# Performance work log

Hardware: AMD Instinct MI355X
Metric: run time of the kernel (lower is better)

The kernel has to match this reference:

```python
import jax, jax.numpy as jnp
import numpy as np


def setup_inputs() -> dict:
    key = jax.random.key(0)
    ks = jax.random.split(key, 8)
    B, C, H, W = 4, 512, 64, 64
    M = C // 8
    sq = 1.0 / np.sqrt(C)
    return {
        "x": jax.random.normal(ks[0], (B, C, H, W), jnp.float32),
        "Wq": jax.random.normal(ks[1], (M, C), jnp.float32) * sq,
        "bq": jnp.zeros((M,), jnp.float32),
        "Wk": jax.random.normal(ks[2], (M, C), jnp.float32) * sq,
        "bk": jnp.zeros((M,), jnp.float32),
        "Wv": jax.random.normal(ks[3], (C, C), jnp.float32) * sq,
        "bv": jnp.zeros((C,), jnp.float32),
        "gamma": jax.random.uniform(ks[4], (1,), jnp.float32),
    }


def reference(x, Wq, bq, Wk, bk, Wv, bv, gamma):
    B, C, H, W = x.shape
    N = H * W
    xf = x.reshape(B, C, N)  # flatten spatial -> [B, C, N]
    # 1x1 convs are channel-mixing matmuls
    q = jnp.einsum('mc,bcn->bmn', Wq, xf) + bq[None, :, None]  # [B, M, N]
    k = jnp.einsum('mc,bcn->bmn', Wk, xf) + bk[None, :, None]  # [B, M, N]
    v = jnp.einsum('dc,bcn->bdn', Wv, xf) + bv[None, :, None]  # [B, C, N]
    # sim[b,i,j] = <q[:, i], k[:, j]>, softmax over j
    sim = jnp.einsum('bmi,bmj->bij', q, k)  # [B, N, N]
    attn = jax.nn.softmax(sim, axis=-1)
    # feat[b,c,i] = sum_j v[b,c,j] * attn[b,i,j]
    feat = jnp.einsum('bcj,bij->bci', v, attn)  # [B, C, N]
    out = gamma[0] * feat.reshape(B, C, H, W) + x
    return out
```

## Files before the change

### kernel.cpp

```cpp
#include <hip/hip_runtime.h>

typedef _Float16 f16;
typedef _Float16 f16x8 __attribute__((ext_vector_type(8)));
typedef float    f32x4 __attribute__((ext_vector_type(4)));
typedef unsigned int u32x2 __attribute__((ext_vector_type(2)));

#define B_ 4
#define C_ 512
#define N_ 4096
#define M_ 64

__device__ __forceinline__ unsigned pk2(float a, float b) {
    union { f16 h[2]; unsigned u; } t;
    t.h[0] = (f16)a; t.h[1] = (f16)b;
    return t.u;
}

__global__ __launch_bounds__(256) void wcvt(
    const float* __restrict__ Wq, const float* __restrict__ Wk,
    const float* __restrict__ Wv, f16* __restrict__ Wf)
{
    const int e = (blockIdx.x * 256 + threadIdx.x) * 8;
    const float* src;
    int off;
    if (e < 32768)      { src = Wq; off = e; }
    else if (e < 65536) { src = Wk; off = e - 32768; }
    else                { src = Wv; off = e - 65536; }
    float4 a = *(const float4*)(src + off);
    float4 b = *(const float4*)(src + off + 4);
    f16x8 o;
    o[0]=(f16)a.x; o[1]=(f16)a.y; o[2]=(f16)a.z; o[3]=(f16)a.w;
    o[4]=(f16)b.x; o[5]=(f16)b.y; o[6]=(f16)b.z; o[7]=(f16)b.w;
    *(f16x8*)(Wf + e) = o;
}

__global__ __launch_bounds__(512) void qkv2(
    const f16* __restrict__ Wf, const float* __restrict__ x,
    const float* __restrict__ bq, const float* __restrict__ bk,
    const float* __restrict__ bv,
    f16* __restrict__ qt, f16* __restrict__ ktf, f16* __restrict__ vf)
{
    __shared__ __align__(16) char sH[2][8192];
    __shared__ float sBias[640];

    const int tid  = threadIdx.x;
    const int w    = tid >> 6;
    const int lane = tid & 63;
    const int l15  = lane & 15;
    const int quad = lane >> 4;
    const int n0   = blockIdx.x * 64;
    const int b    = blockIdx.y;
    const int row0 = w * 80;

    for (int e = tid; e < 640; e += 512)
        sBias[e] = (e < 64) ? bq[e] : (e < 128) ? bk[e - 64] : bv[e - 128];

    const int wbyte = (lane * 128 + w * 16) ^ ((lane & 7) << 4);
    int rbyte[4][2];
    #pragma unroll
    for (int nt = 0; nt < 4; ++nt) {
        const int n = nt * 16 + l15;
        #pragma unroll
        for (int kh = 0; kh < 2; ++kh)
            rbyte[nt][kh] = (n * 128 + kh * 64 + quad * 16) ^ ((n & 7) << 4);
    }

    const float* xg = x + (size_t)b * (C_ * N_) + n0 + lane;
    const f16*   wp = Wf + (size_t)row0 * 512 + quad * 8;

    {
        float g[8];
        #pragma unroll
        for (int u = 0; u < 8; ++u)
            g[u] = xg[(size_t)(w * 8 + u) * N_];
        f16x8 h;
        #pragma unroll
        for (int u = 0; u < 8; ++u) h[u] = (f16)g[u];
        *(f16x8*)(&sH[0][0] + wbyte) = h;
    }
    f16x8 afc[5][2];
    #pragma unroll
    for (int ot = 0; ot < 5; ++ot)
        #pragma unroll
        for (int kh = 0; kh < 2; ++kh)
            afc[ot][kh] = *(const f16x8*)(wp + (size_t)(ot * 16 + l15) * 512 + kh * 32);

    f32x4 acc[5][4] = {};

    for (int t = 0; t < 8; ++t) {
        char* sc = &sH[t & 1][0];
        char* sn = &sH[(t & 1) ^ 1][0];

        float gn[8];
        f16x8 afn[5][2];
        if (t < 7) {
            #pragma unroll
            for (int u = 0; u < 8; ++u)
                gn[u] = xg[(size_t)((t + 1) * 64 + w * 8 + u) * N_];
            #pragma unroll
            for (int ot = 0; ot < 5; ++ot)
                #pragma unroll
                for (int kh = 0; kh < 2; ++kh)
                    afn[ot][kh] = *(const f16x8*)(wp + (size_t)(ot * 16 + l15) * 512
                                                  + (t + 1) * 64 + kh * 32);
        }

        __syncthreads();

        f16x8 bf[4][2];
        #pragma unroll
        for (int nt = 0; nt < 4; ++nt)
            #pragma unroll
            for (int kh = 0; kh < 2; ++kh)
                bf[nt][kh] = *(const f16x8*)(sc + rbyte[nt][kh]);

        #pragma unroll
        for (int ot = 0; ot < 5; ++ot)
            #pragma unroll
            for (int kh = 0; kh < 2; ++kh)
                #pragma unroll
                for (int nt = 0; nt < 4; ++nt)
                    acc[ot][nt] = __builtin_amdgcn_mfma_f32_16x16x32_f16(
                        afc[ot][kh], bf[nt][kh], acc[ot][nt], 0, 0, 0);

        if (t < 7) {
            f16x8 h;
            #pragma unroll
            for (int u = 0; u < 8; ++u) h[u] = (f16)gn[u];
            *(f16x8*)(sn + wbyte) = h;
            #pragma unroll
            for (int ot = 0; ot < 5; ++ot)
                #pragma unroll
                for (int kh = 0; kh < 2; ++kh)
                    afc[ot][kh] = afn[ot][kh];
        }
    }

    #pragma unroll
    for (int ot = 0; ot < 5; ++ot) {
        const int rowBase = row0 + ot * 16;
        const int rq = rowBase + quad * 4;
        #pragma unroll
        for (int nt = 0; nt < 4; ++nt) {
            const int n = n0 + nt * 16 + l15;
            union { f16 h[4]; unsigned long long u; } pkv;
            #pragma unroll
            for (int r = 0; r < 4; ++r)
                pkv.h[r] = (f16)(acc[ot][nt][r] + sBias[rq + r]);
            if (rowBase < 64) {
                *(unsigned long long*)(qt + ((size_t)(b * N_ + n)) * M_ + rq) = pkv.u;
            } else if (rowBase < 128) {
                const int ol = rq - 64;
                size_t idx = (((size_t)b * 256 + (n >> 4)) * 2 + (ol >> 5)) * 512
                           + (size_t)((((ol >> 3) & 3) * 16 + (n & 15)) * 8) + (ol & 7);
                *(unsigned long long*)(ktf + idx) = pkv.u;
            } else {
                const int c = rq - 128;
                #pragma unroll
                for (int r = 0; r < 4; ++r) {
                    size_t idx = ((size_t)b * (C_ * N_)) + (size_t)((c + r) >> 4) * 65536
                               + (size_t)(n >> 6) * 1024 + (size_t)((n >> 5) & 1) * 512
                               + (size_t)((((n >> 3) & 3) * 16 + ((c + r) & 15)) * 8) + (n & 7);
                    vf[idx] = pkv.h[r];
                }
            }
        }
    }
}

__global__ __launch_bounds__(512, 2) void attn(
    const f16* __restrict__ qt, const f16* __restrict__ ktf,
    const f16* __restrict__ vf, const float* __restrict__ x,
    const float* __restrict__ gamma, float* __restrict__ out)
{
    __shared__ __align__(16) char Pb[2][8192];
    __shared__ float mxs[8][4][16];
    __shared__ float lss[8][4][16];

    const int tid  = threadIdx.x;
    const int w    = tid >> 6;
    const int lane = tid & 63;
    const int l15  = lane & 15;
    const int quad = lane >> 4;
    const int jt   = w & 3;
    const int ish  = w >> 2;
    const int is0  = ish * 2, is1 = is0 + 1;

    const int lin  = blockIdx.x;
    const int b    = (lin & 7) >> 1;
    const int iblk = ((lin >> 3) << 1) | (lin & 1);
    const int i0   = iblk * 64;

    const f16* kln = ktf + (size_t)b * (N_ * M_) + lane * 8;
    const f16* vln = vf  + (size_t)b * (C_ * N_) + lane * 8;

    f16x8 bqf[4][2];
    #pragma unroll
    for (int is = 0; is < 4; ++is)
        #pragma unroll
        for (int kh = 0; kh < 2; ++kh)
            bqf[is][kh] = *(const f16x8*)(qt + ((size_t)(b * N_ + i0 + is * 16 + l15)) * M_
                                          + kh * 32 + quad * 8);

    float mx[4];
    #pragma unroll
    for (int is = 0; is < 4; ++is) mx[is] = -3.0e38f;
    {
        const f16* kw = kln + (size_t)(w * 512) * 64;
        f16x8 akc[4][2];
        #pragma unroll
        for (int t = 0; t < 4; ++t)
            #pragma unroll
            for (int kh = 0; kh < 2; ++kh)
                akc[t][kh] = *(const f16x8*)(kw + t * 1024 + kh * 512);

        #pragma unroll 2
        for (int jj = 0; jj < 512; jj += 64) {
            f16x8 akn[4][2];
            if (jj + 64 < 512) {
                const f16* kn = kw + (size_t)(jj + 64) * 64;
                #pragma unroll
                for (int t = 0; t < 4; ++t)
                    #pragma unroll
                    for (int kh = 0; kh < 2; ++kh)
                        akn[t][kh] = *(const f16x8*)(kn + t * 1024 + kh * 512);
            }
            #pragma unroll
            for (int t = 0; t < 4; ++t) {
                #pragma unroll
                for (int is = 0; is < 4; ++is) {
                    f32x4 s = {};
                    s = __builtin_amdgcn_mfma_f32_16x16x32_f16(akc[t][0], bqf[is][0], s, 0, 0, 0);
                    s = __builtin_amdgcn_mfma_f32_16x16x32_f16(akc[t][1], bqf[is][1], s, 0, 0, 0);
                    mx[is] = fmaxf(mx[is], fmaxf(fmaxf(s[0], s[1]), fmaxf(s[2], s[3])));
                }
            }
            #pragma unroll
            for (int t = 0; t < 4; ++t)
                #pragma unroll
                for (int kh = 0; kh < 2; ++kh)
                    akc[t][kh] = akn[t][kh];
        }
    }
    #pragma unroll
    for (int is = 0; is < 4; ++is) {
        mx[is] = fmaxf(mx[is], __shfl_xor(mx[is], 16, 64));
        mx[is] = fmaxf(mx[is], __shfl_xor(mx[is], 32, 64));
    }
    if (lane < 16) {
        #pragma unroll
        for (int is = 0; is < 4; ++is) mxs[w][is][lane] = mx[is];
    }
    __syncthreads();
    float m0 = -3.0e38f, m1 = -3.0e38f;
    #pragma unroll
    for (int w2 = 0; w2 < 8; ++w2) {
        m0 = fmaxf(m0, mxs[w2][is0][l15]);
        m1 = fmaxf(m1, mxs[w2][is1][l15]);
    }

    f32x4 acc[4][4] = {};
    float lp0 = 0.f, lp1 = 0.f;

    char* pbB = (char*)&Pb[0][0];
    const int swz = (l15 & 7) << 4;
    const int wb0 = ((is0 * 16 + l15) * 128 + (jt * 16 + quad * 4) * 2) ^ swz;
    const int wb1 = wb0 + 2048;
    int rb[4][2];
    #pragma unroll
    for (int is = 0; is < 4; ++is)
        #pragma unroll
        for (int kh = 0; kh < 2; ++kh)
            rb[is][kh] = ((is * 16 + l15) * 128 + kh * 64 + quad * 16) ^ swz;

    const f16* kp = kln + (size_t)(jt * 16) * 64;
    const int cw = w * 4;

    f16x8 ak0 = *(const f16x8*)(kp);
    f16x8 ak1 = *(const f16x8*)(kp + 512);
    {
        f32x4 s0 = {}, s1 = {};
        s0 = __builtin_amdgcn_mfma_f32_16x16x32_f16(ak0, bqf[is0][0], s0, 0, 0, 0);
        s0 = __builtin_amdgcn_mfma_f32_16x16x32_f16(ak1, bqf[is0][1], s0, 0, 0, 0);
        s1 = __builtin_amdgcn_mfma_f32_16x16x32_f16(ak0, bqf[is1][0], s1, 0, 0, 0);
        s1 = __builtin_amdgcn_mfma_f32_16x16x32_f16(ak1, bqf[is1][1], s1, 0, 0, 0);
        float p0 = __expf(s0[0] - m0), p1 = __expf(s0[1] - m0);
        float p2 = __expf(s0[2] - m0), p3 = __expf(s0[3] - m0);
        lp0 += (p0 + p1) + (p2 + p3);
        u32x2 pw0 = { pk2(p0, p1), pk2(p2, p3) };
        *(u32x2*)(pbB + wb0) = pw0;
        float q0 = __expf(s1[0] - m1), q1 = __expf(s1[1] - m1);
        float q2 = __expf(s1[2] - m1), q3 = __expf(s1[3] - m1);
        lp1 += (q0 + q1) + (q2 + q3);
        u32x2 pw1 = { pk2(q0, q1), pk2(q2, q3) };
        *(u32x2*)(pbB + wb1) = pw1;
    }
    ak0 = *(const f16x8*)(kp + 4096);
    ak1 = *(const f16x8*)(kp + 4096 + 512);
    f16x8 vc0[4], vc1[4];
    #pragma unroll
    for (int ct = 0; ct < 4; ++ct) {
        vc0[ct] = *(const f16x8*)(vln + (size_t)(cw + ct) * 65536);
        vc1[ct] = *(const f16x8*)(vln + (size_t)(cw + ct) * 65536 + 512);
    }
    __syncthreads();

    #pragma unroll 2
    for (int t = 0; t < 63; ++t) {
        const int cb = (t & 1) * 8192;
        const int nb = ((t + 1) & 1) * 8192;

        f16x8 pbf[4][2];
        #pragma unroll
        for (int is = 0; is < 4; ++is)
            #pragma unroll
            for (int kh = 0; kh < 2; ++kh)
                pbf[is][kh] = *(const f16x8*)(pbB + cb + rb[is][kh]);

        f32x4 s0 = {}, s1 = {};
        s0 = __builtin_amdgcn_mfma_f32_16x16x32_f16(ak0, bqf[is0][0], s0, 0, 0, 0);
        s0 = __builtin_amdgcn_mfma_f32_16x16x32_f16(ak1, bqf[is0][1], s0, 0, 0, 0);
        s1 = __builtin_amdgcn_mfma_f32_16x16x32_f16(ak0, bqf[is1][0], s1, 0, 0, 0);
        s1 = __builtin_amdgcn_mfma_f32_16x16x32_f16(ak1, bqf[is1][1], s1, 0, 0, 0);

        if (t + 2 < 64) {
            ak0 = *(const f16x8*)(kp + (size_t)(t + 2) * 4096);
            ak1 = *(const f16x8*)(kp + (size_t)(t + 2) * 4096 + 512);
        }
        const f16* vt = vln + (size_t)(t + 1) * 1024;
        f16x8 vn0[4], vn1[4];
        #pragma unroll
        for (int ct = 0; ct < 4; ++ct) {
            vn0[ct] = *(const f16x8*)(vt + (size_t)(cw + ct) * 65536);
            vn1[ct] = *(const f16x8*)(vt + (size_t)(cw + ct) * 65536 + 512);
        }

        {
            float p0 = __expf(s0[0] - m0), p1 = __expf(s0[1] - m0);
            float p2 = __expf(s0[2] - m0), p3 = __expf(s0[3] - m0);
            lp0 += (p0 + p1) + (p2 + p3);
            u32x2 pw = { pk2(p0, p1), pk2(p2, p3) };
            *(u32x2*)(pbB + nb + wb0) = pw;
        }
        {
            float q0 = __expf(s1[0] - m1), q1 = __expf(s1[1] - m1);
            float q2 = __expf(s1[2] - m1), q3 = __expf(s1[3] - m1);
            lp1 += (q0 + q1) + (q2 + q3);
            u32x2 pw = { pk2(q0, q1), pk2(q2, q3) };
            *(u32x2*)(pbB + nb + wb1) = pw;
        }

        __builtin_amdgcn_s_setprio(1);
        #pragma unroll
        for (int ct = 0; ct < 4; ++ct)
            #pragma unroll
            for (int is = 0; is < 4; ++is)
                acc[ct][is] = __builtin_amdgcn_mfma_f32_16x16x32_f16(vc0[ct], pbf[is][0], acc[ct][is], 0, 0, 0);
        #pragma unroll
        for (int ct = 0; ct < 4; ++ct)
            #pragma unroll
            for (int is = 0; is < 4; ++is)
                acc[ct][is] = __builtin_amdgcn_mfma_f32_16x16x32_f16(vc1[ct], pbf[is][1], acc[ct][is], 0, 0, 0);
        __builtin_amdgcn_s_setprio(0);

        __syncthreads();

        #pragma unroll
        for (int ct = 0; ct < 4; ++ct) { vc0[ct] = vn0[ct]; vc1[ct] = vn1[ct]; }
    }

    {
        const int cb = (63 & 1) * 8192;
        f16x8 pbf[4][2];
        #pragma unroll
        for (int is = 0; is < 4; ++is)
            #pragma unroll
            for (int kh = 0; kh < 2; ++kh)
                pbf[is][kh] = *(const f16x8*)(pbB + cb + rb[is][kh]);
        #pragma unroll
        for (int ct = 0; ct < 4; ++ct)
            #pragma unroll
            for (int is = 0; is < 4; ++is)
                acc[ct][is] = __builtin_amdgcn_mfma_f32_16x16x32_f16(vc0[ct], pbf[is][0], acc[ct][is], 0, 0, 0);
        #pragma unroll
        for (int ct = 0; ct < 4; ++ct)
            #pragma unroll
            for (int is = 0; is < 4; ++is)
                acc[ct][is] = __builtin_amdgcn_mfma_f32_16x16x32_f16(vc1[ct], pbf[is][1], acc[ct][is], 0, 0, 0);
    }

    lp0 += __shfl_xor(lp0, 16, 64);
    lp0 += __shfl_xor(lp0, 32, 64);
    lp1 += __shfl_xor(lp1, 16, 64);
    lp1 += __shfl_xor(lp1, 32, 64);
    if (lane < 16) { lss[w][is0][lane] = lp0; lss[w][is1][lane] = lp1; }
    __syncthreads();

    float linv[4];
    #pragma unroll
    for (int is = 0; is < 4; ++is) {
        const int wb = (is >> 1) * 4;
        float l = (lss[wb + 0][is][l15] + lss[wb + 1][is][l15])
                + (lss[wb + 2][is][l15] + lss[wb + 3][is][l15]);
        linv[is] = 1.0f / l;
    }

    const float g = gamma[0];
    #pragma unroll
    for (int is = 0; is < 4; ++is) {
        const int i = i0 + is * 16 + l15;
        #pragma unroll
        for (int ct = 0; ct < 4; ++ct) {
            #pragma unroll
            for (int r = 0; r < 4; ++r) {
                const int c = w * 64 + ct * 16 + quad * 4 + r;
                const size_t idx = ((size_t)(b * C_ + c)) * N_ + i;
                out[idx] = g * (acc[ct][is][r] * linv[is]) + x[idx];
            }
        }
    }
}

extern "C" void kernel_launch(void* const* d_in, const int* in_sizes, int n_in,
                              void* d_out, int out_size, void* d_ws, size_t ws_size,
                              hipStream_t stream)
{
    const float* x     = (const float*)d_in[0];
    const float* Wq    = (const float*)d_in[1];
    const float* bq    = (const float*)d_in[2];
    const float* Wk    = (const float*)d_in[3];
    const float* bk    = (const float*)d_in[4];
    const float* Wv    = (const float*)d_in[5];
    const float* bv    = (const float*)d_in[6];
    const float* gamma = (const float*)d_in[7];
    float* out = (float*)d_out;

    char* ws = (char*)d_ws;
    f16* qt  = (f16*)ws;
    f16* ktf = qt + (size_t)B_ * N_ * M_;
    f16* vf  = ktf + (size_t)B_ * N_ * M_;
    f16* Wf  = vf + (size_t)B_ * C_ * N_;

    wcvt<<<dim3(160), 256, 0, stream>>>(Wq, Wk, Wv, Wf);
    qkv2<<<dim3(N_ / 64, B_), 512, 0, stream>>>(Wf, x, bq, bk, bv, qt, ktf, vf);
    attn<<<dim3(256), 512, 0, stream>>>(qt, ktf, vf, x, gamma, out);
}
```

Baseline: 215.2 us.

## Triple-buffer QKV projection smem and ping-pong attention register buffers

The QKV projection kernel moves to a three-stage shared-memory ring with x prefetched two tiles ahead. Weight fragments are now loaded per iteration instead of being double-buffered in registers, and launch bounds request two blocks per CU. The attention loop is manually unrolled by two through a macro that ping-pongs K and V register buffers, which removes the register copies, and __syncthreads is replaced with an explicit lgkmcnt wait, s_barrier and sched_barrier. The aim is to cut register-move overhead and improve latency hiding, at the risk of extra register pressure or spills and weaker compiler scheduling.

Result: slower. 219.9 us (+2.2%).

```diff
diff --git a/kernel.cpp b/kernel.cpp
--- a/kernel.cpp
+++ b/kernel.cpp
@@ -34,13 +34,13 @@
     *(f16x8*)(Wf + e) = o;
 }
 
-__global__ __launch_bounds__(512) void qkv2(
+__global__ __launch_bounds__(512, 2) void qkv4(
     const f16* __restrict__ Wf, const float* __restrict__ x,
     const float* __restrict__ bq, const float* __restrict__ bk,
     const float* __restrict__ bv,
     f16* __restrict__ qt, f16* __restrict__ ktf, f16* __restrict__ vf)
 {
-    __shared__ __align__(16) char sH[2][8192];
+    __shared__ __align__(16) char sH[3][8192];
     __shared__ float sBias[640];
 
     const int tid  = threadIdx.x;
@@ -58,55 +58,48 @@
     const int wbyte = (lane * 128 + w * 16) ^ ((lane & 7) << 4);
     int rbyte[4][2];
     #pragma unroll
-    for (int nt = 0; nt < 4; ++nt) {
-        const int n = nt * 16 + l15;
+    for (int nt = 0; nt < 4; ++nt)
         #pragma unroll
         for (int kh = 0; kh < 2; ++kh)
-            rbyte[nt][kh] = (n * 128 + kh * 64 + quad * 16) ^ ((n & 7) << 4);
-    }
+            rbyte[nt][kh] = ((nt * 16 + l15) * 128 + kh * 64 + quad * 16)
+                            ^ ((l15 & 7) << 4);
 
     const float* xg = x + (size_t)b * (C_ * N_) + n0 + lane;
     const f16*   wp = Wf + (size_t)row0 * 512 + quad * 8;
 
+    float gn[2][8];
     {
-        float g[8];
-        #pragma unroll
-        for (int u = 0; u < 8; ++u)
-            g[u] = xg[(size_t)(w * 8 + u) * N_];
+        float g0[8];
+        #pragma unroll
+        for (int u = 0; u < 8; ++u) g0[u] = xg[(size_t)(w * 8 + u) * N_];
+        #pragma unroll
+        for (int u = 0; u < 8; ++u) gn[1][u] = xg[(size_t)(64 + w * 8 + u) * N_];
         f16x8 h;
         #pragma unroll
-        for (int u = 0; u < 8; ++u) h[u] = (f16)g[u];
+        for (int u = 0; u < 8; ++u) h[u] = (f16)g0[u];
         *(f16x8*)(&sH[0][0] + wbyte) = h;
     }
-    f16x8 afc[5][2];
-    #pragma unroll
-    for (int ot = 0; ot < 5; ++ot)
-        #pragma unroll
-        for (int kh = 0; kh < 2; ++kh)
-            afc[ot][kh] = *(const f16x8*)(wp + (size_t)(ot * 16 + l15) * 512 + kh * 32);
+    asm volatile("s_waitcnt lgkmcnt(0)" ::: "memory");
+    __builtin_amdgcn_s_barrier();
+    __builtin_amdgcn_sched_barrier(0);
 
     f32x4 acc[5][4] = {};
 
+    #pragma unroll
     for (int t = 0; t < 8; ++t) {
-        char* sc = &sH[t & 1][0];
-        char* sn = &sH[(t & 1) ^ 1][0];
-
-        float gn[8];
-        f16x8 afn[5][2];
-        if (t < 7) {
+        f16x8 af[5][2];
+        #pragma unroll
+        for (int ot = 0; ot < 5; ++ot)
+            #pragma unroll
+            for (int kh = 0; kh < 2; ++kh)
+                af[ot][kh] = *(const f16x8*)(wp + (size_t)(ot * 16 + l15) * 512
+                                             + t * 64 + kh * 32);
+        if (t + 2 < 8) {
             #pragma unroll
             for (int u = 0; u < 8; ++u)
-                gn[u] = xg[(size_t)((t + 1) * 64 + w * 8 + u) * N_];
-            #pragma unroll
-            for (int ot = 0; ot < 5; ++ot)
-                #pragma unroll
-                for (int kh = 0; kh < 2; ++kh)
-                    afn[ot][kh] = *(const f16x8*)(wp + (size_t)(ot * 16 + l15) * 512
-                                                  + (t + 1) * 64 + kh * 32);
+                gn[t & 1][u] = xg[(size_t)((t + 2) * 64 + w * 8 + u) * N_];
         }
-
-        __syncthreads();
-
+        const char* sc = &sH[t % 3][0];
         f16x8 bf[4][2];
         #pragma unroll
         for (int nt = 0; nt < 4; ++nt)
@@ -121,19 +114,17 @@
                 #pragma unroll
                 for (int nt = 0; nt < 4; ++nt)
                     acc[ot][nt] = __builtin_amdgcn_mfma_f32_16x16x32_f16(
-                        afc[ot][kh], bf[nt][kh], acc[ot][nt], 0, 0, 0);
-
-        if (t < 7) {
+                        af[ot][kh], bf[nt][kh], acc[ot][nt], 0, 0, 0);
+
+        if (t + 1 < 8) {
             f16x8 h;
             #pragma unroll
-            for (int u = 0; u < 8; ++u) h[u] = (f16)gn[u];
-            *(f16x8*)(sn + wbyte) = h;
-            #pragma unroll
-            for (int ot = 0; ot < 5; ++ot)
-                #pragma unroll
-                for (int kh = 0; kh < 2; ++kh)
-                    afc[ot][kh] = afn[ot][kh];
+            for (int u = 0; u < 8; ++u) h[u] = (f16)gn[(t + 1) & 1][u];
+            *(f16x8*)(&sH[(t + 1) % 3][0] + wbyte) = h;
         }
+        asm volatile("s_waitcnt lgkmcnt(0)" ::: "memory");
+        __builtin_amdgcn_s_barrier();
+        __builtin_amdgcn_sched_barrier(0);
     }
 
     #pragma unroll
@@ -276,14 +267,17 @@
     const f16* kp = kln + (size_t)(jt * 16) * 64;
     const int cw = w * 4;
 
-    f16x8 ak0 = *(const f16x8*)(kp);
-    f16x8 ak1 = *(const f16x8*)(kp + 512);
+    f16x8 akr[2][2];
+    f16x8 vr[2][8];
+
+    akr[0][0] = *(const f16x8*)(kp);
+    akr[0][1] = *(const f16x8*)(kp + 512);
     {
         f32x4 s0 = {}, s1 = {};
-        s0 = __builtin_amdgcn_mfma_f32_16x16x32_f16(ak0, bqf[is0][0], s0, 0, 0, 0);
-        s0 = __builtin_amdgcn_mfma_f32_16x16x32_f16(ak1, bqf[is0][1], s0, 0, 0, 0);
-        s1 = __builtin_amdgcn_mfma_f32_16x16x32_f16(ak0, bqf[is1][0], s1, 0, 0, 0);
-        s1 = __builtin_amdgcn_mfma_f32_16x16x32_f16(ak1, bqf[is1][1], s1, 0, 0, 0);
+        s0 = __builtin_amdgcn_mfma_f32_16x16x32_f16(akr[0][0], bqf[is0][0], s0, 0, 0, 0);
+        s0 = __builtin_amdgcn_mfma_f32_16x16x32_f16(akr[0][1], bqf[is0][1], s0, 0, 0, 0);
+        s1 = __builtin_amdgcn_mfma_f32_16x16x32_f16(akr[0][0], bqf[is1][0], s1, 0, 0, 0);
+        s1 = __builtin_amdgcn_mfma_f32_16x16x32_f16(akr[0][1], bqf[is1][1], s1, 0, 0, 0);
         float p0 = __expf(s0[0] - m0), p1 = __expf(s0[1] - m0);
         float p2 = __expf(s0[2] - m0), p3 = __expf(s0[3] - m0);
         lp0 += (p0 + p1) + (p2 + p3);
@@ -295,98 +289,96 @@
         u32x2 pw1 = { pk2(q0, q1), pk2(q2, q3) };
         *(u32x2*)(pbB + wb1) = pw1;
     }
-    ak0 = *(const f16x8*)(kp + 4096);
-    ak1 = *(const f16x8*)(kp + 4096 + 512);
-    f16x8 vc0[4], vc1[4];
+    akr[1][0] = *(const f16x8*)(kp + 4096);
+    akr[1][1] = *(const f16x8*)(kp + 4096 + 512);
     #pragma unroll
     for (int ct = 0; ct < 4; ++ct) {
-        vc0[ct] = *(const f16x8*)(vln + (size_t)(cw + ct) * 65536);
-        vc1[ct] = *(const f16x8*)(vln + (size_t)(cw + ct) * 65536 + 512);
+        vr[0][ct]     = *(const f16x8*)(vln + (size_t)(cw + ct) * 65536);
+        vr[0][ct + 4] = *(const f16x8*)(vln + (size_t)(cw + ct) * 65536 + 512);
     }
     __syncthreads();
 
-    #pragma unroll 2
-    for (int t = 0; t < 63; ++t) {
-        const int cb = (t & 1) * 8192;
-        const int nb = ((t + 1) & 1) * 8192;
-
+#define ATTN_BODY(T, CBc, NBc) {                                              \
+    f16x8 pbf[4][2];                                                          \
+    _Pragma("unroll")                                                         \
+    for (int is_ = 0; is_ < 4; ++is_)                                         \
+        _Pragma("unroll")                                                     \
+        for (int kh_ = 0; kh_ < 2; ++kh_)                                     \
+            pbf[is_][kh_] = *(const f16x8*)(pbB + (CBc) * 8192 + rb[is_][kh_]); \
+    f32x4 s0 = {}, s1 = {};                                                   \
+    s0 = __builtin_amdgcn_mfma_f32_16x16x32_f16(akr[NBc][0], bqf[is0][0], s0, 0, 0, 0); \
+    s0 = __builtin_amdgcn_mfma_f32_16x16x32_f16(akr[NBc][1], bqf[is0][1], s0, 0, 0, 0); \
+    s1 = __builtin_amdgcn_mfma_f32_16x16x32_f16(akr[NBc][0], bqf[is1][0], s1, 0, 0, 0); \
+    s1 = __builtin_amdgcn_mfma_f32_16x16x32_f16(akr[NBc][1], bqf[is1][1], s1, 0, 0, 0); \
+    if ((T) + 2 < 64) {                                                       \
+        const f16* kn_ = kp + (size_t)((T) + 2) * 4096;                       \
+        akr[CBc][0] = *(const f16x8*)(kn_);                                   \
+        akr[CBc][1] = *(const f16x8*)(kn_ + 512);                             \
+    }                                                                         \
+    {                                                                         \
+        const f16* vt_ = vln + (size_t)((T) + 1) * 1024;                      \
+        _Pragma("unroll")                                                     \
+        for (int ct_ = 0; ct_ < 4; ++ct_) {                                   \
+            vr[NBc][ct_]     = *(const f16x8*)(vt_ + (size_t)(cw + ct_) * 65536);       \
+            vr[NBc][ct_ + 4] = *(const f16x8*)(vt_ + (size_t)(cw + ct_) * 65536 + 512); \
+        }                                                                     \
+    }                                                                         \
+    {                                                                         \
+        float p0 = __expf(s0[0] - m0), p1 = __expf(s0[1] - m0);               \
+        float p2 = __expf(s0[2] - m0), p3 = __expf(s0[3] - m0);               \
+        lp0 += (p0 + p1) + (p2 + p3);                                         \
+        u32x2 pw = { pk2(p0, p1), pk2(p2, p3) };                              \
+        *(u32x2*)(pbB + (NBc) * 8192 + wb0) = pw;                             \
+    }                                                                         \
+    {                                                                         \
+        float q0 = __expf(s1[0] - m1), q1 = __expf(s1[1] - m1);               \
+        float q2 = __expf(s1[2] - m1), q3 = __expf(s1[3] - m1);               \
+        lp1 += (q0 + q1) + (q2 + q3);                                         \
+        u32x2 pw = { pk2(q0, q1), pk2(q2, q3) };                              \
+        *(u32x2*)(pbB + (NBc) * 8192 + wb1) = pw;                             \
+    }                                                                         \
+    __builtin_amdgcn_s_setprio(1);                                            \
+    _Pragma("unroll")                                                         \
+    for (int ct_ = 0; ct_ < 4; ++ct_)                                         \
+        _Pragma("unroll")                                                     \
+        for (int is_ = 0; is_ < 4; ++is_)                                     \
+            acc[ct_][is_] = __builtin_amdgcn_mfma_f32_16x16x32_f16(           \
+                vr[CBc][ct_], pbf[is_][0], acc[ct_][is_], 0, 0, 0);           \
+    _Pragma("unroll")                                                         \
+    for (int ct_ = 0; ct_ < 4; ++ct_)                                         \
+        _Pragma("unroll")                                                     \
+        for (int is_ = 0; is_ < 4; ++is_)                                     \
+            acc[ct_][is_] = __builtin_amdgcn_mfma_f32_16x16x32_f16(           \
+                vr[CBc][ct_ + 4], pbf[is_][1], acc[ct_][is_], 0, 0, 0);       \
+    __builtin_amdgcn_s_setprio(0);                                            \
+    asm volatile("s_waitcnt lgkmcnt(0)" ::: "memory");                        \
+    __builtin_amdgcn_s_barrier();                                             \
+    __builtin_amdgcn_sched_barrier(0);                                        \
+}
+
+    for (int tt = 0; tt < 62; tt += 2) {
+        ATTN_BODY(tt,     0, 1);
+        ATTN_BODY(tt + 1, 1, 0);
+    }
+    ATTN_BODY(62, 0, 1);
+
+    {
         f16x8 pbf[4][2];
         #pragma unroll
         for (int is = 0; is < 4; ++is)
             #pragma unroll
             for (int kh = 0; kh < 2; ++kh)
-                pbf[is][kh] = *(const f16x8*)(pbB + cb + rb[is][kh]);
-
-        f32x4 s0 = {}, s1 = {};
-        s0 = __builtin_amdgcn_mfma_f32_16x16x32_f16(ak0, bqf[is0][0], s0, 0, 0, 0);
-        s0 = __builtin_amdgcn_mfma_f32_16x16x32_f16(ak1, bqf[is0][1], s0, 0, 0, 0);
-        s1 = __builtin_amdgcn_mfma_f32_16x16x32_f16(ak0, bqf[is1][0], s1, 0, 0, 0);
-        s1 = __builtin_amdgcn_mfma_f32_16x16x32_f16(ak1, bqf[is1][1], s1, 0, 0, 0);
-
-        if (t + 2 < 64) {
-            ak0 = *(const f16x8*)(kp + (size_t)(t + 2) * 4096);
-            ak1 = *(const f16x8*)(kp + (size_t)(t + 2) * 4096 + 512);
-        }
-        const f16* vt = vln + (size_t)(t + 1) * 1024;
-        f16x8 vn0[4], vn1[4];
-        #pragma unroll
-        for (int ct = 0; ct < 4; ++ct) {
-            vn0[ct] = *(const f16x8*)(vt + (size_t)(cw + ct) * 65536);
-            vn1[ct] = *(const f16x8*)(vt + (size_t)(cw + ct) * 65536 + 512);
-        }
-
-        {
-            float p0 = __expf(s0[0] - m0), p1 = __expf(s0[1] - m0);
-            float p2 = __expf(s0[2] - m0), p3 = __expf(s0[3] - m0);
-            lp0 += (p0 + p1) + (p2 + p3);
-            u32x2 pw = { pk2(p0, p1), pk2(p2, p3) };
-            *(u32x2*)(pbB + nb + wb0) = pw;
-        }
-        {
-            float q0 = __expf(s1[0] - m1), q1 = __expf(s1[1] - m1);
-            float q2 = __expf(s1[2] - m1), q3 = __expf(s1[3] - m1);
-            lp1 += (q0 + q1) + (q2 + q3);
-            u32x2 pw = { pk2(q0, q1), pk2(q2, q3) };
-            *(u32x2*)(pbB + nb + wb1) = pw;
-        }
-
-        __builtin_amdgcn_s_setprio(1);
+                pbf[is][kh] = *(const f16x8*)(pbB + 8192 + rb[is][kh]);
         #pragma unroll
         for (int ct = 0; ct < 4; ++ct)
             #pragma unroll
             for (int is = 0; is < 4; ++is)
-                acc[ct][is] = __builtin_amdgcn_mfma_f32_16x16x32_f16(vc0[ct], pbf[is][0], acc[ct][is], 0, 0, 0);
+                acc[ct][is] = __builtin_amdgcn_mfma_f32_16x16x32_f16(vr[1][ct], pbf[is][0], acc[ct][is], 0, 0, 0);
         #pragma unroll
         for (int ct = 0; ct < 4; ++ct)
             #pragma unroll
             for (int is = 0; is < 4; ++is)
-                acc[ct][is] = __builtin_amdgcn_mfma_f32_16x16x32_f16(vc1[ct], pbf[is][1], acc[ct][is], 0, 0, 0);
-        __builtin_amdgcn_s_setprio(0);
-
-        __syncthreads();
-
-        #pragma unroll
-        for (int ct = 0; ct < 4; ++ct) { vc0[ct] = vn0[ct]; vc1[ct] = vn1[ct]; }
-    }
-
-    {
-        const int cb = (63 & 1) * 8192;
-        f16x8 pbf[4][2];
-        #pragma unroll
-        for (int is = 0; is < 4; ++is)
-            #pragma unroll
-            for (int kh = 0; kh < 2; ++kh)
-                pbf[is][kh] = *(const f16x8*)(pbB + cb + rb[is][kh]);
-        #pragma unroll
-        for (int ct = 0; ct < 4; ++ct)
-            #pragma unroll
-            for (int is = 0; is < 4; ++is)
-                acc[ct][is] = __builtin_amdgcn_mfma_f32_16x16x32_f16(vc0[ct], pbf[is][0], acc[ct][is], 0, 0, 0);
-        #pragma unroll
-        for (int ct = 0; ct < 4; ++ct)
-            #pragma unroll
-            for (int is = 0; is < 4; ++is)
-                acc[ct][is] = __builtin_amdgcn_mfma_f32_16x16x32_f16(vc1[ct], pbf[is][1], acc[ct][is], 0, 0, 0);
+                acc[ct][is] = __builtin_amdgcn_mfma_f32_16x16x32_f16(vr[1][ct + 4], pbf[is][1], acc[ct][is], 0, 0, 0);
     }
 
     lp0 += __shfl_xor(lp0, 16, 64);
@@ -442,6 +434,6 @@
     f16* Wf  = vf + (size_t)B_ * C_ * N_;
 
     wcvt<<<dim3(160), 256, 0, stream>>>(Wq, Wk, Wv, Wf);
-    qkv2<<<dim3(N_ / 64, B_), 512, 0, stream>>>(Wf, x, bq, bk, bv, qt, ktf, vf);
+    qkv4<<<dim3(N_ / 64, B_), 512, 0, stream>>>(Wf, x, bq, bk, bv, qt, ktf, vf);
     attn<<<dim3(256), 512, 0, stream>>>(qt, ktf, vf, x, gamma, out);
 }
```
